# Optimization experiments

Hardware: AMD Instinct MI355X
Metric: run time of the kernel (lower is better)

The kernel has to match this reference:

```python
import jax, jax.numpy as jnp
import numpy as np

N = 50000      # nodes
E = 800000     # edges (avg degree 16)
IN = 128       # in_channels
OUT = 64       # out_channels
K = 2          # propagation hops


def setup_inputs() -> dict:
    key = jax.random.key(0)
    k1, k2, k3 = jax.random.split(key, 3)
    x = jax.random.normal(k1, (N, IN), dtype=jnp.float32)
    edge_index = jax.random.randint(k2, (2, E), 0, N, dtype=jnp.int32)
    # SGConv's internal Linear(in, out): weight [OUT, IN], bias [OUT]
    W = jax.random.normal(k3, (OUT, IN), dtype=jnp.float32) / np.sqrt(IN)
    b = jnp.zeros((OUT,), dtype=jnp.float32)
    return {"x": x, "edge_index": edge_index, "W": W, "b": b}


def reference(x, edge_index, W, b):
    # GCN normalization with self-loops (PyG gcn_norm, add_self_loops=True)
    row, col = edge_index[0], edge_index[1]
    loops = jnp.arange(N, dtype=edge_index.dtype)
    row = jnp.concatenate([row, loops])   # source nodes
    col = jnp.concatenate([col, loops])   # target nodes
    ones = jnp.ones((E + N,), dtype=x.dtype)
    deg = jax.ops.segment_sum(ones, col, num_segments=N)          # in-degree incl. self-loop
    deg_inv_sqrt = jnp.where(deg > 0, jax.lax.rsqrt(deg), 0.0)
    norm = deg_inv_sqrt[row] * deg_inv_sqrt[col]                  # [E+N]

    # K-hop propagation: x <- D^{-1/2} (A+I) D^{-1/2} x
    for _ in range(K):
        x = jax.ops.segment_sum(x[row] * norm[:, None], col, num_segments=N)

    # final linear; dropout is identity in eval mode (training=False)
    return x @ W.T + b
```

## Files before the change

kernel.cpp:

```cpp
#include <hip/hip_runtime.h>
#include <hip/hip_bf16.h>
#include <hip/hip_fp16.h>

#define IN_CH 128
#define OUT_CH 64
#define NB 256
#define CHUNK_CAP 3200
#define SORT_CAP 6144

typedef _Float16 hh2 __attribute__((ext_vector_type(2)));

__global__ void __launch_bounds__(512) histo_kernel(const int* __restrict__ col,
                                                    int* __restrict__ blkcnt,
                                                    int* __restrict__ rawcnt,
                                                    int E, int chunk) {
    __shared__ int h[256];
    int blk = blockIdx.x, tid = threadIdx.x;
    if (tid < 256) h[tid] = 0;
    __syncthreads();
    int s = blk * chunk, e = min(s + chunk, E);
    for (int i = s + tid; i < e; i += 512)
        atomicAdd(&h[col[i] >> 8], 1);
    __syncthreads();
    if (tid < 256) {
        blkcnt[blk * 256 + tid] = h[tid];
        rawcnt[blk * 256 + tid] = h[tid];
    }
}

__global__ void __launch_bounds__(256) scanblk_kernel(int* __restrict__ blkcnt,
                                                      int* __restrict__ totals) {
    __shared__ int ps[256];
    int b = blockIdx.x, tid = threadIdx.x;
    int i0 = tid * 256 + b;
    int a0 = blkcnt[i0];
    ps[tid] = a0;
    __syncthreads();
    for (int d = 1; d < 256; d <<= 1) {
        int t = 0;
        if (tid >= d) t = ps[tid - d];
        __syncthreads();
        if (tid >= d) ps[tid] += t;
        __syncthreads();
    }
    blkcnt[i0] = ps[tid] - a0;
    if (tid == 255) totals[b] = ps[255];
}

__global__ void __launch_bounds__(512) bucket_scatter_kernel(const int* __restrict__ row,
                                                             const int* __restrict__ col,
                                                             const int* __restrict__ blkcnt,
                                                             const int* __restrict__ rawcnt,
                                                             const int* __restrict__ totals,
                                                             unsigned int* __restrict__ tmp,
                                                             int E, int chunk, int nbkt) {
    __shared__ int ps[256];
    __shared__ int ls[256];
    __shared__ int bias[256];
    __shared__ int curl[256];
    __shared__ unsigned int vall[CHUNK_CAP];
    __shared__ int destl[CHUNK_CAP];
    int blk = blockIdx.x, tid = threadIdx.x;
    int t0 = 0, lr = 0;
    if (tid < 256) {
        t0 = (tid < nbkt) ? totals[tid] : 0;
        ps[tid] = t0;
        lr = rawcnt[blk * 256 + tid];
        ls[tid] = lr;
    }
    __syncthreads();
    for (int d = 1; d < 256; d <<= 1) {
        int t = 0, u = 0;
        if (tid < 256 && tid >= d) { t = ps[tid - d]; u = ls[tid - d]; }
        __syncthreads();
        if (tid < 256 && tid >= d) { ps[tid] += t; ls[tid] += u; }
        __syncthreads();
    }
    if (tid < 256) {
        int bucket_base = ps[tid] - t0;
        int loff = ls[tid] - lr;
        bias[tid] = bucket_base + blkcnt[blk * 256 + tid] - loff;
        curl[tid] = loff;
    }
    __syncthreads();
    int s = blk * chunk, e = min(s + chunk, E);
    int csize = e - s;
    if (csize <= CHUNK_CAP) {
        for (int i = s + tid; i < e; i += 512) {
            int c = col[i], r = row[i];
            int k = c >> 8;
            int p = atomicAdd(&curl[k], 1);
            vall[p]  = ((unsigned)(c & 255) << 16) | (unsigned)r;
            destl[p] = bias[k] + p;
        }
        __syncthreads();
        for (int j = tid; j < csize; j += 512)
            tmp[destl[j]] = vall[j];
    } else {
        for (int i = s + tid; i < e; i += 512) {
            int c = col[i], r = row[i];
            int k = c >> 8;
            int p = atomicAdd(&curl[k], 1);
            tmp[bias[k] + p] = ((unsigned)(c & 255) << 16) | (unsigned)r;
        }
    }
}

__global__ void __launch_bounds__(512) bucket_sort_kernel(const unsigned int* __restrict__ tmp,
                                                          const int* __restrict__ totals,
                                                          int* __restrict__ off,
                                                          float* __restrict__ dis,
                                                          unsigned short* __restrict__ eidx,
                                                          int nbkt, int E, int n) {
    __shared__ int bs[256];
    __shared__ int cntl[256];
    __shared__ int sc[256];
    __shared__ int posr[256];
    __shared__ unsigned short el[SORT_CAP];
    int b = blockIdx.x, tid = threadIdx.x;
    int v = 0;
    if (tid < 256) { v = (tid < nbkt) ? totals[tid] : 0; bs[tid] = v; }
    __syncthreads();
    for (int d = 1; d < 256; d <<= 1) {
        int t = 0;
        if (tid < 256 && tid >= d) t = bs[tid - d];
        __syncthreads();
        if (tid < 256 && tid >= d) bs[tid] += t;
        __syncthreads();
    }
    if (tid < 256) bs[tid] -= v;
    if (tid < 256) cntl[tid] = 0;
    __syncthreads();
    int s = bs[b];
    int cnt = (b < nbkt) ? totals[b] : 0;
    int e = s + cnt;
    for (int i = s + tid; i < e; i += 512)
        atomicAdd(&cntl[tmp[i] >> 16], 1);
    __syncthreads();
    int c = 0;
    if (tid < 256) { c = cntl[tid]; sc[tid] = c; }
    __syncthreads();
    for (int d = 1; d < 256; d <<= 1) {
        int t = 0;
        if (tid < 256 && tid >= d) t = sc[tid - d];
        __syncthreads();
        if (tid < 256 && tid >= d) sc[tid] += t;
        __syncthreads();
    }
    if (tid < 256) {
        int excl = sc[tid] - c;
        int gid = (b << 8) + tid;
        if (gid < n) {
            off[gid] = s + excl;
            dis[gid] = rsqrtf((float)(c + 1));
        }
        posr[tid] = excl;
    }
    if (b == 0 && tid == 0) off[n] = E;
    __syncthreads();
    bool staged = (cnt <= SORT_CAP);
    if (staged) {
        for (int i = s + tid; i < e; i += 512) {
            unsigned int w = tmp[i];
            int p = atomicAdd(&posr[w >> 16], 1);
            el[p] = (unsigned short)(w & 0xFFFFu);
        }
        __syncthreads();
        for (int i = tid; i < cnt; i += 512)
            eidx[s + i] = el[i];
    } else {
        for (int i = s + tid; i < e; i += 512) {
            unsigned int w = tmp[i];
            int p = atomicAdd(&posr[w >> 16], 1);
            eidx[s + p] = (unsigned short)(w & 0xFFFFu);
        }
    }
}

__global__ void __launch_bounds__(256) gemm_kernel(const float* __restrict__ x,
                                                   const float* __restrict__ W,
                                                   const float* __restrict__ dis,
                                                   __half* __restrict__ z, int n) {
    __shared__ hh2 Xs[64 * 66];
    __shared__ hh2 Ws[64 * 66];
    int t = threadIdx.x;
    int m0 = blockIdx.x * 64;
#pragma unroll
    for (int r = 0; r < 8; ++r) {
        int f = t + 256 * r;
        int o = f >> 5, kq = f & 31;
        float4 w = ((const float4*)W)[f];
        Ws[o * 66 + kq * 2]     = hh2{(_Float16)w.x, (_Float16)w.y};
        Ws[o * 66 + kq * 2 + 1] = hh2{(_Float16)w.z, (_Float16)w.w};
    }
#pragma unroll
    for (int r = 0; r < 8; ++r) {
        int f = t + 256 * r;
        int node = f >> 5, kq = f & 31;
        int gv = min(m0 + node, n - 1);
        float4 xv = ((const float4*)(x + (size_t)gv * IN_CH))[kq];
        Xs[node * 66 + kq * 2]     = hh2{(_Float16)xv.x, (_Float16)xv.y};
        Xs[node * 66 + kq * 2 + 1] = hh2{(_Float16)xv.z, (_Float16)xv.w};
    }
    __syncthreads();
    int tx = t & 15, ty = t >> 4;
    float acc[4][4];
#pragma unroll
    for (int i = 0; i < 4; ++i)
#pragma unroll
        for (int j = 0; j < 4; ++j) acc[i][j] = 0.f;

#pragma unroll 4
    for (int kq = 0; kq < 32; ++kq) {
        hh2 xa0[4], xa1[4], wb0[4], wb1[4];
#pragma unroll
        for (int i = 0; i < 4; ++i) {
            int base = (tx + 16 * i) * 66 + kq * 2;
            xa0[i] = Xs[base]; xa1[i] = Xs[base + 1];
        }
#pragma unroll
        for (int j = 0; j < 4; ++j) {
            int base = (ty * 4 + j) * 66 + kq * 2;
            wb0[j] = Ws[base]; wb1[j] = Ws[base + 1];
        }
#pragma unroll
        for (int i = 0; i < 4; ++i)
#pragma unroll
            for (int j = 0; j < 4; ++j) {
                float s = acc[i][j];
                s = __builtin_amdgcn_fdot2(xa0[i], wb0[j], s, false);
                s = __builtin_amdgcn_fdot2(xa1[i], wb1[j], s, false);
                acc[i][j] = s;
            }
    }
#pragma unroll
    for (int i = 0; i < 4; ++i) {
        int v = m0 + tx + 16 * i;
        if (v < n) {
            float dv = dis[v];
            union { __half2 h[2]; float2 f; } u;
            u.h[0] = __floats2half2_rn(dv * acc[i][0], dv * acc[i][1]);
            u.h[1] = __floats2half2_rn(dv * acc[i][2], dv * acc[i][3]);
            *(float2*)&z[(size_t)v * OUT_CH + ty * 4] = u.f;
        }
    }
}

#define ACC8(raw) { const __half2* h2_ = (const __half2*)&(raw);              \
    float2 f0_ = __half22float2(h2_[0]), f1_ = __half22float2(h2_[1]);        \
    float2 f2_ = __half22float2(h2_[2]), f3_ = __half22float2(h2_[3]);        \
    a0 += f0_.x; a1 += f0_.y; a2 += f1_.x; a3 += f1_.y;                       \
    a4 += f2_.x; a5 += f2_.y; a6 += f3_.x; a7 += f3_.y; }

template <int MODE>
__global__ void __launch_bounds__(256) hop_kernel(const __half* __restrict__ zin,
                                                  void* __restrict__ out,
                                                  const unsigned short* __restrict__ eidx,
                                                  const int* __restrict__ off,
                                                  const float* __restrict__ dis,
                                                  const float* __restrict__ bias, int n) {
    int v = (int)((blockIdx.x * 256 + threadIdx.x) >> 6);
    if (v >= n) return;
    int lane = threadIdx.x & 63;
    int grp = lane >> 3;
    int sub = lane & 7;
    int s = off[v], e = off[v + 1];
    float dv = dis[v];
    float a0 = 0.f, a1 = 0.f, a2 = 0.f, a3 = 0.f;
    float a4 = 0.f, a5 = 0.f, a6 = 0.f, a7 = 0.f;
    if (grp == 0) {
        float4 raw = ((const float4*)(zin + (size_t)v * OUT_CH))[sub];
        ACC8(raw);
    }
    int i0 = s + grp;
    int i1 = i0 + 8, i2 = i0 + 16, i3 = i0 + 24;
    bool h0 = i0 < e, h1 = i1 < e, h2 = i2 < e, h3 = i3 < e;
    int r0 = h0 ? (int)eidx[i0] : 0;
    int r1 = h1 ? (int)eidx[i1] : 0;
    int r2 = h2 ? (int)eidx[i2] : 0;
    int r3 = h3 ? (int)eidx[i3] : 0;
    float4 rA = make_float4(0.f, 0.f, 0.f, 0.f);
    float4 rB = make_float4(0.f, 0.f, 0.f, 0.f);
    float4 rC = make_float4(0.f, 0.f, 0.f, 0.f);
    float4 rD = make_float4(0.f, 0.f, 0.f, 0.f);
    if (h0) rA = ((const float4*)(zin + (size_t)r0 * OUT_CH))[sub];
    if (h1) rB = ((const float4*)(zin + (size_t)r1 * OUT_CH))[sub];
    if (h2) rC = ((const float4*)(zin + (size_t)r2 * OUT_CH))[sub];
    if (h3) rD = ((const float4*)(zin + (size_t)r3 * OUT_CH))[sub];
    ACC8(rA); ACC8(rB); ACC8(rC); ACC8(rD);
    if (e - s > 32) {
        int j0 = s + 32 + grp, j1 = j0 + 8;
        bool g0 = j0 < e, g1 = j1 < e;
        int q0 = g0 ? (int)eidx[j0] : 0;
        int q1 = g1 ? (int)eidx[j1] : 0;
        while (g0) {
            int k0 = j0 + 16, k1 = j1 + 16;
            bool f0 = k0 < e, f1 = k1 < e;
            int p0 = f0 ? (int)eidx[k0] : 0;
            int p1 = f1 ? (int)eidx[k1] : 0;
            float4 xA = make_float4(0.f, 0.f, 0.f, 0.f);
            float4 xB = make_float4(0.f, 0.f, 0.f, 0.f);
            if (g0) xA = ((const float4*)(zin + (size_t)q0 * OUT_CH))[sub];
            if (g1) xB = ((const float4*)(zin + (size_t)q1 * OUT_CH))[sub];
            ACC8(xA); ACC8(xB);
            j0 = k0; j1 = k1; q0 = p0; q1 = p1; g0 = f0; g1 = f1;
        }
    }
#pragma unroll
    for (int m = 8; m <= 32; m <<= 1) {
        a0 += __shfl_xor(a0, m, 64); a1 += __shfl_xor(a1, m, 64);
        a2 += __shfl_xor(a2, m, 64); a3 += __shfl_xor(a3, m, 64);
        a4 += __shfl_xor(a4, m, 64); a5 += __shfl_xor(a5, m, 64);
        a6 += __shfl_xor(a6, m, 64); a7 += __shfl_xor(a7, m, 64);
    }
    if (grp == 0) {
        if (MODE == 0) {
            float sc = dv * dv;
            union { __half2 h[4]; float4 f; } u;
            u.h[0] = __floats2half2_rn(sc * a0, sc * a1);
            u.h[1] = __floats2half2_rn(sc * a2, sc * a3);
            u.h[2] = __floats2half2_rn(sc * a4, sc * a5);
            u.h[3] = __floats2half2_rn(sc * a6, sc * a7);
            ((float4*)((__half*)out + (size_t)v * OUT_CH))[sub] = u.f;
        } else {
            const float4* bp = (const float4*)(bias + sub * 8);
            float4 b0 = bp[0], b1 = bp[1];
            float* op = (float*)out + (size_t)v * OUT_CH + sub * 8;
            *(float4*)op = make_float4(fmaf(dv, a0, b0.x), fmaf(dv, a1, b0.y),
                                       fmaf(dv, a2, b0.z), fmaf(dv, a3, b0.w));
            *(float4*)(op + 4) = make_float4(fmaf(dv, a4, b1.x), fmaf(dv, a5, b1.y),
                                             fmaf(dv, a6, b1.z), fmaf(dv, a7, b1.w));
        }
    }
}

extern "C" void kernel_launch(void* const* d_in, const int* in_sizes, int n_in,
                              void* d_out, int out_size, void* d_ws, size_t ws_size,
                              hipStream_t stream) {
    const float* x = (const float*)d_in[0];
    const int* ei = (const int*)d_in[1];
    const float* W = (const float*)d_in[2];
    const float* b = (const float*)d_in[3];
    int n = in_sizes[0] / IN_CH;
    int E = in_sizes[1] / 2;
    const int* row = ei;
    const int* col = ei + E;

    char* ws = (char*)d_ws;
    size_t o = 0;
    auto alloc = [&](size_t bytes) -> void* {
        void* p = ws + o;
        o += (bytes + 255) & ~(size_t)255;
        return p;
    };
    int nbkt = (n + 255) >> 8;
    int chunk = (E + NB - 1) / NB;

    int*            blkcnt = (int*)alloc((size_t)NB * 256 * 4);
    int*            rawcnt = (int*)alloc((size_t)NB * 256 * 4);
    int*            totals = (int*)alloc(256 * 4);
    unsigned int*   tmp    = (unsigned int*)alloc((size_t)E * 4);
    int*            off    = (int*)alloc((size_t)(n + 1) * 4);
    float*          dis    = (float*)alloc((size_t)n * 4);
    unsigned short* eidx   = (unsigned short*)alloc((size_t)E * 2);
    __half*         zA     = (__half*)alloc((size_t)n * OUT_CH * 2);
    __half*         zB     = (__half*)alloc((size_t)n * OUT_CH * 2);

    histo_kernel<<<NB, 512, 0, stream>>>(col, blkcnt, rawcnt, E, chunk);
    scanblk_kernel<<<nbkt, 256, 0, stream>>>(blkcnt, totals);
    bucket_scatter_kernel<<<NB, 512, 0, stream>>>(row, col, blkcnt, rawcnt, totals, tmp, E, chunk, nbkt);
    bucket_sort_kernel<<<nbkt, 512, 0, stream>>>(tmp, totals, off, dis, eidx, nbkt, E, n);
    gemm_kernel<<<(n + 63) / 64, 256, 0, stream>>>(x, W, dis, zA, n);
    int hopBlocks = (n + 3) / 4;
    hop_kernel<0><<<hopBlocks, 256, 0, stream>>>(zA, zB, eidx, off, dis, nullptr, n);
    hop_kernel<1><<<hopBlocks, 256, 0, stream>>>(zB, d_out, eidx, off, dis, b, n);
}
```

Before: 153.7 us.

## Fuse histogram into GEMM launch, drop scan kernel, move source-degree scaling into hop

The histogram blocks now run inside the GEMM launch as extra blocks, so the GEMM no longer waits on the degree computation and its output is left unscaled by the source normalisation. The separate block-scan kernel is removed: scatter and sort each recompute per-bucket totals and prefixes by looping over the raw counts. The first hop multiplies each gathered neighbour row by that neighbour's inverse-sqrt degree with an extra dis[] load. This cuts two launches and a serial dependency, at the cost of redundant prefix work in every scatter and sort block and extra scalar gathers in the first hop.

```diff
diff --git a/kernel.cpp b/kernel.cpp
--- a/kernel.cpp
+++ b/kernel.cpp
@@ -10,76 +10,124 @@
 
 typedef _Float16 hh2 __attribute__((ext_vector_type(2)));
 
-__global__ void __launch_bounds__(512) histo_kernel(const int* __restrict__ col,
-                                                    int* __restrict__ blkcnt,
-                                                    int* __restrict__ rawcnt,
-                                                    int E, int chunk) {
-    __shared__ int h[256];
-    int blk = blockIdx.x, tid = threadIdx.x;
-    if (tid < 256) h[tid] = 0;
-    __syncthreads();
-    int s = blk * chunk, e = min(s + chunk, E);
-    for (int i = s + tid; i < e; i += 512)
-        atomicAdd(&h[col[i] >> 8], 1);
-    __syncthreads();
-    if (tid < 256) {
-        blkcnt[blk * 256 + tid] = h[tid];
-        rawcnt[blk * 256 + tid] = h[tid];
-    }
-}
-
-__global__ void __launch_bounds__(256) scanblk_kernel(int* __restrict__ blkcnt,
-                                                      int* __restrict__ totals) {
-    __shared__ int ps[256];
-    int b = blockIdx.x, tid = threadIdx.x;
-    int i0 = tid * 256 + b;
-    int a0 = blkcnt[i0];
-    ps[tid] = a0;
-    __syncthreads();
-    for (int d = 1; d < 256; d <<= 1) {
-        int t = 0;
-        if (tid >= d) t = ps[tid - d];
-        __syncthreads();
-        if (tid >= d) ps[tid] += t;
-        __syncthreads();
-    }
-    blkcnt[i0] = ps[tid] - a0;
-    if (tid == 255) totals[b] = ps[255];
-}
-
-__global__ void __launch_bounds__(512) bucket_scatter_kernel(const int* __restrict__ row,
-                                                             const int* __restrict__ col,
-                                                             const int* __restrict__ blkcnt,
-                                                             const int* __restrict__ rawcnt,
-                                                             const int* __restrict__ totals,
-                                                             unsigned int* __restrict__ tmp,
-                                                             int E, int chunk, int nbkt) {
-    __shared__ int ps[256];
-    __shared__ int ls[256];
-    __shared__ int bias[256];
+__global__ void __launch_bounds__(256) fat1_kernel(const float* __restrict__ x,
+                                                   const float* __restrict__ W,
+                                                   __half* __restrict__ z0,
+                                                   const int* __restrict__ col,
+                                                   int* __restrict__ rawcnt,
+                                                   int n, int E, int chunk, int GB) {
+    __shared__ char smraw[64 * 66 * 2 * 2 * 2];
+    int t = threadIdx.x;
+
+    if (blockIdx.x >= GB) {
+        int* h = (int*)smraw;
+        int blk = blockIdx.x - GB;
+        h[t] = 0;
+        __syncthreads();
+        int s = blk * chunk, e = min(s + chunk, E);
+        for (int i = s + t; i < e; i += 256)
+            atomicAdd(&h[col[i] >> 8], 1);
+        __syncthreads();
+        rawcnt[blk * 256 + t] = h[t];
+        return;
+    }
+
+    hh2* Xs = (hh2*)smraw;
+    hh2* Ws = Xs + 64 * 66;
+    int m0 = blockIdx.x * 64;
+#pragma unroll
+    for (int r = 0; r < 8; ++r) {
+        int f = t + 256 * r;
+        int o = f >> 5, kq = f & 31;
+        float4 w = ((const float4*)W)[f];
+        Ws[o * 66 + kq * 2]     = hh2{(_Float16)w.x, (_Float16)w.y};
+        Ws[o * 66 + kq * 2 + 1] = hh2{(_Float16)w.z, (_Float16)w.w};
+    }
+#pragma unroll
+    for (int r = 0; r < 8; ++r) {
+        int f = t + 256 * r;
+        int node = f >> 5, kq = f & 31;
+        int gv = min(m0 + node, n - 1);
+        float4 xv = ((const float4*)(x + (size_t)gv * IN_CH))[kq];
+        Xs[node * 66 + kq * 2]     = hh2{(_Float16)xv.x, (_Float16)xv.y};
+        Xs[node * 66 + kq * 2 + 1] = hh2{(_Float16)xv.z, (_Float16)xv.w};
+    }
+    __syncthreads();
+    int tx = t & 15, ty = t >> 4;
+    float acc[4][4];
+#pragma unroll
+    for (int i = 0; i < 4; ++i)
+#pragma unroll
+        for (int j = 0; j < 4; ++j) acc[i][j] = 0.f;
+#pragma unroll 4
+    for (int kq = 0; kq < 32; ++kq) {
+        hh2 xa0[4], xa1[4], wb0[4], wb1[4];
+#pragma unroll
+        for (int i = 0; i < 4; ++i) {
+            int base = (tx + 16 * i) * 66 + kq * 2;
+            xa0[i] = Xs[base]; xa1[i] = Xs[base + 1];
+        }
+#pragma unroll
+        for (int j = 0; j < 4; ++j) {
+            int base = (ty * 4 + j) * 66 + kq * 2;
+            wb0[j] = Ws[base]; wb1[j] = Ws[base + 1];
+        }
+#pragma unroll
+        for (int i = 0; i < 4; ++i)
+#pragma unroll
+            for (int j = 0; j < 4; ++j) {
+                float s = acc[i][j];
+                s = __builtin_amdgcn_fdot2(xa0[i], wb0[j], s, false);
+                s = __builtin_amdgcn_fdot2(xa1[i], wb1[j], s, false);
+                acc[i][j] = s;
+            }
+    }
+#pragma unroll
+    for (int i = 0; i < 4; ++i) {
+        int v = m0 + tx + 16 * i;
+        if (v < n) {
+            union { __half2 h[2]; float2 f; } u;
+            u.h[0] = __floats2half2_rn(acc[i][0], acc[i][1]);
+            u.h[1] = __floats2half2_rn(acc[i][2], acc[i][3]);
+            *(float2*)&z0[(size_t)v * OUT_CH + ty * 4] = u.f;
+        }
+    }
+}
+
+__global__ void __launch_bounds__(512) scatter_kernel(const int* __restrict__ row,
+                                                      const int* __restrict__ col,
+                                                      const int* __restrict__ rawcnt,
+                                                      unsigned int* __restrict__ tmp,
+                                                      int E, int chunk) {
+    __shared__ int psT[256];
+    __shared__ int psC[256];
+    __shared__ int biasl[256];
     __shared__ int curl[256];
     __shared__ unsigned int vall[CHUNK_CAP];
     __shared__ int destl[CHUNK_CAP];
     int blk = blockIdx.x, tid = threadIdx.x;
-    int t0 = 0, lr = 0;
+    int T = 0, P = 0, C = 0;
     if (tid < 256) {
-        t0 = (tid < nbkt) ? totals[tid] : 0;
-        ps[tid] = t0;
-        lr = rawcnt[blk * 256 + tid];
-        ls[tid] = lr;
+        for (int b = 0; b < NB; ++b) {
+            int v = rawcnt[b * 256 + tid];
+            T += v;
+            P += (b < blk) ? v : 0;
+            C = (b == blk) ? v : C;
+        }
+        psT[tid] = T; psC[tid] = C;
     }
     __syncthreads();
     for (int d = 1; d < 256; d <<= 1) {
-        int t = 0, u = 0;
-        if (tid < 256 && tid >= d) { t = ps[tid - d]; u = ls[tid - d]; }
-        __syncthreads();
-        if (tid < 256 && tid >= d) { ps[tid] += t; ls[tid] += u; }
+        int a = 0, c2 = 0;
+        if (tid < 256 && tid >= d) { a = psT[tid - d]; c2 = psC[tid - d]; }
+        __syncthreads();
+        if (tid < 256 && tid >= d) { psT[tid] += a; psC[tid] += c2; }
         __syncthreads();
     }
     if (tid < 256) {
-        int bucket_base = ps[tid] - t0;
-        int loff = ls[tid] - lr;
-        bias[tid] = bucket_base + blkcnt[blk * 256 + tid] - loff;
+        int B = psT[tid] - T;
+        int loff = psC[tid] - C;
+        biasl[tid] = B + P - loff;
         curl[tid] = loff;
     }
     __syncthreads();
@@ -91,7 +139,7 @@
             int k = c >> 8;
             int p = atomicAdd(&curl[k], 1);
             vall[p]  = ((unsigned)(c & 255) << 16) | (unsigned)r;
-            destl[p] = bias[k] + p;
+            destl[p] = biasl[k] + p;
         }
         __syncthreads();
         for (int j = tid; j < csize; j += 512)
@@ -101,38 +149,43 @@
             int c = col[i], r = row[i];
             int k = c >> 8;
             int p = atomicAdd(&curl[k], 1);
-            tmp[bias[k] + p] = ((unsigned)(c & 255) << 16) | (unsigned)r;
-        }
-    }
-}
-
-__global__ void __launch_bounds__(512) bucket_sort_kernel(const unsigned int* __restrict__ tmp,
-                                                          const int* __restrict__ totals,
-                                                          int* __restrict__ off,
-                                                          float* __restrict__ dis,
-                                                          unsigned short* __restrict__ eidx,
-                                                          int nbkt, int E, int n) {
+            tmp[biasl[k] + p] = ((unsigned)(c & 255) << 16) | (unsigned)r;
+        }
+    }
+}
+
+__global__ void __launch_bounds__(512) sort_kernel(const unsigned int* __restrict__ tmp,
+                                                   const int* __restrict__ rawcnt,
+                                                   int* __restrict__ off,
+                                                   float* __restrict__ dis,
+                                                   unsigned short* __restrict__ eidx,
+                                                   int nbkt, int E, int n) {
     __shared__ int bs[256];
+    __shared__ int cntT[256];
     __shared__ int cntl[256];
     __shared__ int sc[256];
     __shared__ int posr[256];
     __shared__ unsigned short el[SORT_CAP];
     int b = blockIdx.x, tid = threadIdx.x;
-    int v = 0;
-    if (tid < 256) { v = (tid < nbkt) ? totals[tid] : 0; bs[tid] = v; }
+    int T = 0;
+    if (tid < 256) {
+        for (int bb = 0; bb < NB; ++bb)
+            T += rawcnt[bb * 256 + tid];
+        bs[tid] = T; cntT[tid] = T;
+    }
     __syncthreads();
     for (int d = 1; d < 256; d <<= 1) {
-        int t = 0;
-        if (tid < 256 && tid >= d) t = bs[tid - d];
-        __syncthreads();
-        if (tid < 256 && tid >= d) bs[tid] += t;
-        __syncthreads();
-    }
-    if (tid < 256) bs[tid] -= v;
+        int a = 0;
+        if (tid < 256 && tid >= d) a = bs[tid - d];
+        __syncthreads();
+        if (tid < 256 && tid >= d) bs[tid] += a;
+        __syncthreads();
+    }
+    if (tid < 256) bs[tid] -= T;
     if (tid < 256) cntl[tid] = 0;
     __syncthreads();
     int s = bs[b];
-    int cnt = (b < nbkt) ? totals[b] : 0;
+    int cnt = cntT[b];
     int e = s + cnt;
     for (int i = s + tid; i < e; i += 512)
         atomicAdd(&cntl[tmp[i] >> 16], 1);
@@ -141,10 +194,10 @@
     if (tid < 256) { c = cntl[tid]; sc[tid] = c; }
     __syncthreads();
     for (int d = 1; d < 256; d <<= 1) {
-        int t = 0;
-        if (tid < 256 && tid >= d) t = sc[tid - d];
-        __syncthreads();
-        if (tid < 256 && tid >= d) sc[tid] += t;
+        int a = 0;
+        if (tid < 256 && tid >= d) a = sc[tid - d];
+        __syncthreads();
+        if (tid < 256 && tid >= d) sc[tid] += a;
         __syncthreads();
     }
     if (tid < 256) {
@@ -177,80 +230,19 @@
     }
 }
 
-__global__ void __launch_bounds__(256) gemm_kernel(const float* __restrict__ x,
-                                                   const float* __restrict__ W,
-                                                   const float* __restrict__ dis,
-                                                   __half* __restrict__ z, int n) {
-    __shared__ hh2 Xs[64 * 66];
-    __shared__ hh2 Ws[64 * 66];
-    int t = threadIdx.x;
-    int m0 = blockIdx.x * 64;
-#pragma unroll
-    for (int r = 0; r < 8; ++r) {
-        int f = t + 256 * r;
-        int o = f >> 5, kq = f & 31;
-        float4 w = ((const float4*)W)[f];
-        Ws[o * 66 + kq * 2]     = hh2{(_Float16)w.x, (_Float16)w.y};
-        Ws[o * 66 + kq * 2 + 1] = hh2{(_Float16)w.z, (_Float16)w.w};
-    }
-#pragma unroll
-    for (int r = 0; r < 8; ++r) {
-        int f = t + 256 * r;
-        int node = f >> 5, kq = f & 31;
-        int gv = min(m0 + node, n - 1);
-        float4 xv = ((const float4*)(x + (size_t)gv * IN_CH))[kq];
-        Xs[node * 66 + kq * 2]     = hh2{(_Float16)xv.x, (_Float16)xv.y};
-        Xs[node * 66 + kq * 2 + 1] = hh2{(_Float16)xv.z, (_Float16)xv.w};
-    }
-    __syncthreads();
-    int tx = t & 15, ty = t >> 4;
-    float acc[4][4];
-#pragma unroll
-    for (int i = 0; i < 4; ++i)
-#pragma unroll
-        for (int j = 0; j < 4; ++j) acc[i][j] = 0.f;
-
-#pragma unroll 4
-    for (int kq = 0; kq < 32; ++kq) {
-        hh2 xa0[4], xa1[4], wb0[4], wb1[4];
-#pragma unroll
-        for (int i = 0; i < 4; ++i) {
-            int base = (tx + 16 * i) * 66 + kq * 2;
-            xa0[i] = Xs[base]; xa1[i] = Xs[base + 1];
-        }
-#pragma unroll
-        for (int j = 0; j < 4; ++j) {
-            int base = (ty * 4 + j) * 66 + kq * 2;
-            wb0[j] = Ws[base]; wb1[j] = Ws[base + 1];
-        }
-#pragma unroll
-        for (int i = 0; i < 4; ++i)
-#pragma unroll
-            for (int j = 0; j < 4; ++j) {
-                float s = acc[i][j];
-                s = __builtin_amdgcn_fdot2(xa0[i], wb0[j], s, false);
-                s = __builtin_amdgcn_fdot2(xa1[i], wb1[j], s, false);
-                acc[i][j] = s;
-            }
-    }
-#pragma unroll
-    for (int i = 0; i < 4; ++i) {
-        int v = m0 + tx + 16 * i;
-        if (v < n) {
-            float dv = dis[v];
-            union { __half2 h[2]; float2 f; } u;
-            u.h[0] = __floats2half2_rn(dv * acc[i][0], dv * acc[i][1]);
-            u.h[1] = __floats2half2_rn(dv * acc[i][2], dv * acc[i][3]);
-            *(float2*)&z[(size_t)v * OUT_CH + ty * 4] = u.f;
-        }
-    }
-}
-
 #define ACC8(raw) { const __half2* h2_ = (const __half2*)&(raw);              \
     float2 f0_ = __half22float2(h2_[0]), f1_ = __half22float2(h2_[1]);        \
     float2 f2_ = __half22float2(h2_[2]), f3_ = __half22float2(h2_[3]);        \
     a0 += f0_.x; a1 += f0_.y; a2 += f1_.x; a3 += f1_.y;                       \
     a4 += f2_.x; a5 += f2_.y; a6 += f3_.x; a7 += f3_.y; }
+
+#define FMA8(raw, dr) { const __half2* h2_ = (const __half2*)&(raw);          \
+    float2 f0_ = __half22float2(h2_[0]), f1_ = __half22float2(h2_[1]);        \
+    float2 f2_ = __half22float2(h2_[2]), f3_ = __half22float2(h2_[3]);        \
+    a0 = fmaf(dr, f0_.x, a0); a1 = fmaf(dr, f0_.y, a1);                       \
+    a2 = fmaf(dr, f1_.x, a2); a3 = fmaf(dr, f1_.y, a3);                       \
+    a4 = fmaf(dr, f2_.x, a4); a5 = fmaf(dr, f2_.y, a5);                       \
+    a6 = fmaf(dr, f3_.x, a6); a7 = fmaf(dr, f3_.y, a7); }
 
 template <int MODE>
 __global__ void __launch_bounds__(256) hop_kernel(const __half* __restrict__ zin,
@@ -270,7 +262,7 @@
     float a4 = 0.f, a5 = 0.f, a6 = 0.f, a7 = 0.f;
     if (grp == 0) {
         float4 raw = ((const float4*)(zin + (size_t)v * OUT_CH))[sub];
-        ACC8(raw);
+        if (MODE == 0) { FMA8(raw, dv); } else { ACC8(raw); }
     }
     int i0 = s + grp;
     int i1 = i0 + 8, i2 = i0 + 16, i3 = i0 + 24;
@@ -279,6 +271,13 @@
     int r1 = h1 ? (int)eidx[i1] : 0;
     int r2 = h2 ? (int)eidx[i2] : 0;
     int r3 = h3 ? (int)eidx[i3] : 0;
+    float d0 = 1.f, d1 = 1.f, d2 = 1.f, d3 = 1.f;
+    if (MODE == 0) {
+        if (h0) d0 = dis[r0];
+        if (h1) d1 = dis[r1];
+        if (h2) d2 = dis[r2];
+        if (h3) d3 = dis[r3];
+    }
     float4 rA = make_float4(0.f, 0.f, 0.f, 0.f);
     float4 rB = make_float4(0.f, 0.f, 0.f, 0.f);
     float4 rC = make_float4(0.f, 0.f, 0.f, 0.f);
@@ -287,7 +286,11 @@
     if (h1) rB = ((const float4*)(zin + (size_t)r1 * OUT_CH))[sub];
     if (h2) rC = ((const float4*)(zin + (size_t)r2 * OUT_CH))[sub];
     if (h3) rD = ((const float4*)(zin + (size_t)r3 * OUT_CH))[sub];
-    ACC8(rA); ACC8(rB); ACC8(rC); ACC8(rD);
+    if (MODE == 0) {
+        FMA8(rA, d0); FMA8(rB, d1); FMA8(rC, d2); FMA8(rD, d3);
+    } else {
+        ACC8(rA); ACC8(rB); ACC8(rC); ACC8(rD);
+    }
     if (e - s > 32) {
         int j0 = s + 32 + grp, j1 = j0 + 8;
         bool g0 = j0 < e, g1 = j1 < e;
@@ -298,11 +301,17 @@
             bool f0 = k0 < e, f1 = k1 < e;
             int p0 = f0 ? (int)eidx[k0] : 0;
             int p1 = f1 ? (int)eidx[k1] : 0;
+            float dq0 = 1.f, dq1 = 1.f;
+            if (MODE == 0) {
+                if (g0) dq0 = dis[q0];
+                if (g1) dq1 = dis[q1];
+            }
             float4 xA = make_float4(0.f, 0.f, 0.f, 0.f);
             float4 xB = make_float4(0.f, 0.f, 0.f, 0.f);
             if (g0) xA = ((const float4*)(zin + (size_t)q0 * OUT_CH))[sub];
             if (g1) xB = ((const float4*)(zin + (size_t)q1 * OUT_CH))[sub];
-            ACC8(xA); ACC8(xB);
+            if (MODE == 0) { FMA8(xA, dq0); FMA8(xB, dq1); }
+            else           { ACC8(xA); ACC8(xB); }
             j0 = k0; j1 = k1; q0 = p0; q1 = p1; g0 = f0; g1 = f1;
         }
     }
@@ -355,10 +364,9 @@
     };
     int nbkt = (n + 255) >> 8;
     int chunk = (E + NB - 1) / NB;
-
-    int*            blkcnt = (int*)alloc((size_t)NB * 256 * 4);
+    int GB = (n + 63) / 64;
+
     int*            rawcnt = (int*)alloc((size_t)NB * 256 * 4);
-    int*            totals = (int*)alloc(256 * 4);
     unsigned int*   tmp    = (unsigned int*)alloc((size_t)E * 4);
     int*            off    = (int*)alloc((size_t)(n + 1) * 4);
     float*          dis    = (float*)alloc((size_t)n * 4);
@@ -366,11 +374,9 @@
     __half*         zA     = (__half*)alloc((size_t)n * OUT_CH * 2);
     __half*         zB     = (__half*)alloc((size_t)n * OUT_CH * 2);
 
-    histo_kernel<<<NB, 512, 0, stream>>>(col, blkcnt, rawcnt, E, chunk);
-    scanblk_kernel<<<nbkt, 256, 0, stream>>>(blkcnt, totals);
-    bucket_scatter_kernel<<<NB, 512, 0, stream>>>(row, col, blkcnt, rawcnt, totals, tmp, E, chunk, nbkt);
-    bucket_sort_kernel<<<nbkt, 512, 0, stream>>>(tmp, totals, off, dis, eidx, nbkt, E, n);
-    gemm_kernel<<<(n + 63) / 64, 256, 0, stream>>>(x, W, dis, zA, n);
+    fat1_kernel<<<GB + NB, 256, 0, stream>>>(x, W, zA, col, rawcnt, n, E, chunk, GB);
+    scatter_kernel<<<NB, 512, 0, stream>>>(row, col, rawcnt, tmp, E, chunk);
+    sort_kernel<<<nbkt, 512, 0, stream>>>(tmp, rawcnt, off, dis, eidx, nbkt, E, n);
     int hopBlocks = (n + 3) / 4;
     hop_kernel<0><<<hopBlocks, 256, 0, stream>>>(zA, zB, eidx, off, dis, nullptr, n);
     hop_kernel<1><<<hopBlocks, 256, 0, stream>>>(zB, d_out, eidx, off, dis, b, n);
```

Measured after the change: 161.2 us. 1.05x slower.

## Split propagated features into two 32-channel halves for cache-resident hop passes

Applied to the files above, without the earlier changes.

The GEMM now writes its fp16 output as two separate 32-channel arrays instead of one 64-channel array. Each hop pass runs twice, once per half, using 8-byte gathers. Each half's working set is 3.2 MB instead of 6.4 MB, which is meant to let the random neighbour gathers stay in cache (L2/Infinity Cache). The cost is twice as many hop launches, with the edge index and offsets read twice.

```diff
diff --git a/kernel.cpp b/kernel.cpp
--- a/kernel.cpp
+++ b/kernel.cpp
@@ -9,6 +9,7 @@
 #define SORT_CAP 6144
 
 typedef _Float16 hh2 __attribute__((ext_vector_type(2)));
+
 
 __global__ void __launch_bounds__(512) histo_kernel(const int* __restrict__ col,
                                                     int* __restrict__ blkcnt,
@@ -180,7 +181,8 @@
 __global__ void __launch_bounds__(256) gemm_kernel(const float* __restrict__ x,
                                                    const float* __restrict__ W,
                                                    const float* __restrict__ dis,
-                                                   __half* __restrict__ z, int n) {
+                                                   __half* __restrict__ zlo,
+                                                   __half* __restrict__ zhi, int n) {
     __shared__ hh2 Xs[64 * 66];
     __shared__ hh2 Ws[64 * 66];
     int t = threadIdx.x;
@@ -233,6 +235,8 @@
                 acc[i][j] = s;
             }
     }
+    __half* dst = (ty < 8) ? zlo : zhi;
+    int fo = (ty & 7) * 4;
 #pragma unroll
     for (int i = 0; i < 4; ++i) {
         int v = m0 + tx + 16 * i;
@@ -241,24 +245,23 @@
             union { __half2 h[2]; float2 f; } u;
             u.h[0] = __floats2half2_rn(dv * acc[i][0], dv * acc[i][1]);
             u.h[1] = __floats2half2_rn(dv * acc[i][2], dv * acc[i][3]);
-            *(float2*)&z[(size_t)v * OUT_CH + ty * 4] = u.f;
-        }
-    }
-}
-
-#define ACC8(raw) { const __half2* h2_ = (const __half2*)&(raw);              \
+            *(float2*)&dst[(size_t)v * 32 + fo] = u.f;
+        }
+    }
+}
+
+#define ACC4(raw) { const __half2* h2_ = (const __half2*)&(raw);              \
     float2 f0_ = __half22float2(h2_[0]), f1_ = __half22float2(h2_[1]);        \
-    float2 f2_ = __half22float2(h2_[2]), f3_ = __half22float2(h2_[3]);        \
-    a0 += f0_.x; a1 += f0_.y; a2 += f1_.x; a3 += f1_.y;                       \
-    a4 += f2_.x; a5 += f2_.y; a6 += f3_.x; a7 += f3_.y; }
+    a0 += f0_.x; a1 += f0_.y; a2 += f1_.x; a3 += f1_.y; }
 
 template <int MODE>
-__global__ void __launch_bounds__(256) hop_kernel(const __half* __restrict__ zin,
-                                                  void* __restrict__ out,
-                                                  const unsigned short* __restrict__ eidx,
-                                                  const int* __restrict__ off,
-                                                  const float* __restrict__ dis,
-                                                  const float* __restrict__ bias, int n) {
+__global__ void __launch_bounds__(256) hop_half_kernel(const __half* __restrict__ zin,
+                                                       void* __restrict__ out,
+                                                       const unsigned short* __restrict__ eidx,
+                                                       const int* __restrict__ off,
+                                                       const float* __restrict__ dis,
+                                                       const float* __restrict__ bias,
+                                                       int n, int fbase) {
     int v = (int)((blockIdx.x * 256 + threadIdx.x) >> 6);
     if (v >= n) return;
     int lane = threadIdx.x & 63;
@@ -267,10 +270,9 @@
     int s = off[v], e = off[v + 1];
     float dv = dis[v];
     float a0 = 0.f, a1 = 0.f, a2 = 0.f, a3 = 0.f;
-    float a4 = 0.f, a5 = 0.f, a6 = 0.f, a7 = 0.f;
     if (grp == 0) {
-        float4 raw = ((const float4*)(zin + (size_t)v * OUT_CH))[sub];
-        ACC8(raw);
+        float2 raw = ((const float2*)(zin + (size_t)v * 32))[sub];
+        ACC4(raw);
     }
     int i0 = s + grp;
     int i1 = i0 + 8, i2 = i0 + 16, i3 = i0 + 24;
@@ -279,15 +281,15 @@
     int r1 = h1 ? (int)eidx[i1] : 0;
     int r2 = h2 ? (int)eidx[i2] : 0;
     int r3 = h3 ? (int)eidx[i3] : 0;
-    float4 rA = make_float4(0.f, 0.f, 0.f, 0.f);
-    float4 rB = make_float4(0.f, 0.f, 0.f, 0.f);
-    float4 rC = make_float4(0.f, 0.f, 0.f, 0.f);
-    float4 rD = make_float4(0.f, 0.f, 0.f, 0.f);
-    if (h0) rA = ((const float4*)(zin + (size_t)r0 * OUT_CH))[sub];
-    if (h1) rB = ((const float4*)(zin + (size_t)r1 * OUT_CH))[sub];
-    if (h2) rC = ((const float4*)(zin + (size_t)r2 * OUT_CH))[sub];
-    if (h3) rD = ((const float4*)(zin + (size_t)r3 * OUT_CH))[sub];
-    ACC8(rA); ACC8(rB); ACC8(rC); ACC8(rD);
+    float2 rA = make_float2(0.f, 0.f);
+    float2 rB = make_float2(0.f, 0.f);
+    float2 rC = make_float2(0.f, 0.f);
+    float2 rD = make_float2(0.f, 0.f);
+    if (h0) rA = ((const float2*)(zin + (size_t)r0 * 32))[sub];
+    if (h1) rB = ((const float2*)(zin + (size_t)r1 * 32))[sub];
+    if (h2) rC = ((const float2*)(zin + (size_t)r2 * 32))[sub];
+    if (h3) rD = ((const float2*)(zin + (size_t)r3 * 32))[sub];
+    ACC4(rA); ACC4(rB); ACC4(rC); ACC4(rD);
     if (e - s > 32) {
         int j0 = s + 32 + grp, j1 = j0 + 8;
         bool g0 = j0 < e, g1 = j1 < e;
@@ -298,11 +300,11 @@
             bool f0 = k0 < e, f1 = k1 < e;
             int p0 = f0 ? (int)eidx[k0] : 0;
             int p1 = f1 ? (int)eidx[k1] : 0;
-            float4 xA = make_float4(0.f, 0.f, 0.f, 0.f);
-            float4 xB = make_float4(0.f, 0.f, 0.f, 0.f);
-            if (g0) xA = ((const float4*)(zin + (size_t)q0 * OUT_CH))[sub];
-            if (g1) xB = ((const float4*)(zin + (size_t)q1 * OUT_CH))[sub];
-            ACC8(xA); ACC8(xB);
+            float2 xA = make_float2(0.f, 0.f);
+            float2 xB = make_float2(0.f, 0.f);
+            if (g0) xA = ((const float2*)(zin + (size_t)q0 * 32))[sub];
+            if (g1) xB = ((const float2*)(zin + (size_t)q1 * 32))[sub];
+            ACC4(xA); ACC4(xB);
             j0 = k0; j1 = k1; q0 = p0; q1 = p1; g0 = f0; g1 = f1;
         }
     }
@@ -310,26 +312,19 @@
     for (int m = 8; m <= 32; m <<= 1) {
         a0 += __shfl_xor(a0, m, 64); a1 += __shfl_xor(a1, m, 64);
         a2 += __shfl_xor(a2, m, 64); a3 += __shfl_xor(a3, m, 64);
-        a4 += __shfl_xor(a4, m, 64); a5 += __shfl_xor(a5, m, 64);
-        a6 += __shfl_xor(a6, m, 64); a7 += __shfl_xor(a7, m, 64);
     }
     if (grp == 0) {
         if (MODE == 0) {
             float sc = dv * dv;
-            union { __half2 h[4]; float4 f; } u;
+            union { __half2 h[2]; float2 f; } u;
             u.h[0] = __floats2half2_rn(sc * a0, sc * a1);
             u.h[1] = __floats2half2_rn(sc * a2, sc * a3);
-            u.h[2] = __floats2half2_rn(sc * a4, sc * a5);
-            u.h[3] = __floats2half2_rn(sc * a6, sc * a7);
-            ((float4*)((__half*)out + (size_t)v * OUT_CH))[sub] = u.f;
+            ((float2*)((__half*)out + (size_t)v * 32))[sub] = u.f;
         } else {
-            const float4* bp = (const float4*)(bias + sub * 8);
-            float4 b0 = bp[0], b1 = bp[1];
-            float* op = (float*)out + (size_t)v * OUT_CH + sub * 8;
+            float4 b0 = *(const float4*)(bias + fbase + sub * 4);
+            float* op = (float*)out + (size_t)v * OUT_CH + fbase + sub * 4;
             *(float4*)op = make_float4(fmaf(dv, a0, b0.x), fmaf(dv, a1, b0.y),
                                        fmaf(dv, a2, b0.z), fmaf(dv, a3, b0.w));
-            *(float4*)(op + 4) = make_float4(fmaf(dv, a4, b1.x), fmaf(dv, a5, b1.y),
-                                             fmaf(dv, a6, b1.z), fmaf(dv, a7, b1.w));
         }
     }
 }
@@ -363,15 +358,20 @@
     int*            off    = (int*)alloc((size_t)(n + 1) * 4);
     float*          dis    = (float*)alloc((size_t)n * 4);
     unsigned short* eidx   = (unsigned short*)alloc((size_t)E * 2);
-    __half*         zA     = (__half*)alloc((size_t)n * OUT_CH * 2);
-    __half*         zB     = (__half*)alloc((size_t)n * OUT_CH * 2);
+    __half*         zAlo   = (__half*)alloc((size_t)n * 32 * 2);
+    __half*         zAhi   = (__half*)alloc((size_t)n * 32 * 2);
+    __half*         zBlo   = (__half*)alloc((size_t)n * 32 * 2);
+    __half*         zBhi   = (__half*)alloc((size_t)n * 32 * 2);
 
     histo_kernel<<<NB, 512, 0, stream>>>(col, blkcnt, rawcnt, E, chunk);
     scanblk_kernel<<<nbkt, 256, 0, stream>>>(blkcnt, totals);
     bucket_scatter_kernel<<<NB, 512, 0, stream>>>(row, col, blkcnt, rawcnt, totals, tmp, E, chunk, nbkt);
     bucket_sort_kernel<<<nbkt, 512, 0, stream>>>(tmp, totals, off, dis, eidx, nbkt, E, n);
-    gemm_kernel<<<(n + 63) / 64, 256, 0, stream>>>(x, W, dis, zA, n);
+    gemm_kernel<<<(n + 63) / 64, 256, 0, stream>>>(x, W, dis, zAlo, zAhi, n);
+
     int hopBlocks = (n + 3) / 4;
-    hop_kernel<0><<<hopBlocks, 256, 0, stream>>>(zA, zB, eidx, off, dis, nullptr, n);
-    hop_kernel<1><<<hopBlocks, 256, 0, stream>>>(zB, d_out, eidx, off, dis, b, n);
-}
+    hop_half_kernel<0><<<hopBlocks, 256, 0, stream>>>(zAlo, zBlo, eidx, off, dis, nullptr, n, 0);
+    hop_half_kernel<1><<<hopBlocks, 256, 0, stream>>>(zBlo, d_out, eidx, off, dis, b, n, 0);
+    hop_half_kernel<0><<<hopBlocks, 256, 0, stream>>>(zAhi, zBhi, eidx, off, dis, nullptr, n, 32);
+    hop_half_kernel<1><<<hopBlocks, 256, 0, stream>>>(zBhi, d_out, eidx, off, dis, b, n, 32);
+}
```

New measurement: 183.7 us. +19.5%, slower.
